# Kernel optimization log

Measured on AMD Instinct MI355X. Metric: run time of the kernel, lower is better.

## Reference

```python
import jax, jax.numpy as jnp
import numpy as np

# DPLayer config (init kwargs)
MAX_OP = False            # False -> min-plus (shortest path) semiring; null = +inf
MAKE_POS = True           # GraphLayer make_pos: force positive edge weights
NULL = -1e30 if MAX_OP else 1e30   # finite stand-in for +/-inf (grad-safe)
B, H, W = 512, 256, 256


def setup_inputs() -> dict:
    key = jax.random.key(0)
    images = jax.random.normal(key, (B, 1, H, W), dtype=jnp.float32)
    return {"images": images}


def _edge_weights(images):
    # GraphLayer: edge_f('euclidean') on pixel values, made positive via softplus.
    x = images[:, 0, :, :]                       # [B, H, W] node/edge costs theta
    if MAKE_POS:
        x = jax.nn.softplus(x)
    return x


def _dp(theta):
    # V[i,j] = theta[i,j] + comb(V[i-1,j], V[i-1,j-1], V[i,j-1]); comb = min (max_op=False)
    # Row recurrence is solved in parallel via prefix-sum + associative running-min:
    #   A[j] = comb(V[i-1,j], V[i-1,j-1])
    #   V[i,j] = S[j] + runmin_{k<=j}(A[k] - S[k-1]),  S = cumsum(theta row)
    comb = jnp.maximum if MAX_OP else jnp.minimum
    null = jnp.asarray(NULL, theta.dtype)
    b = theta.shape[0]

    v0 = jnp.cumsum(theta[:, 0, :], axis=-1)     # first row: only right moves

    def row_step(vprev, th_row):                 # vprev: [B,W], th_row: [B,W]
        shifted = jnp.concatenate([jnp.full((b, 1), null, theta.dtype), vprev[:, :-1]], axis=1)
        A = comb(vprev, shifted)                 # best of up / up-left
        S = jnp.cumsum(th_row, axis=-1)
        Sprev = jnp.concatenate([jnp.zeros((b, 1), theta.dtype), S[:, :-1]], axis=1)
        V = S + jax.lax.associative_scan(comb, A - Sprev, axis=-1)
        return V, None

    vlast, _ = jax.lax.scan(row_step, v0, jnp.moveaxis(theta[:, 1:, :], 1, 0))
    return vlast[:, -1]                          # path length to (H-1, W-1), [B]


def reference(images):
    theta = _edge_weights(images)
    fake_lengths = _dp(theta)
    return fake_lengths
```

## Files before the change

kernel.cpp:

```cpp
#include <hip/hip_runtime.h>


#define HH 256
#define WW 256
#define CH 32
#define NCH 8
#define NULLV 1e30f

#define SBAR() __builtin_amdgcn_sched_barrier(0)

template<int CTRL, int ROWM>
__device__ __forceinline__ float dpp_mov(float x, float oldv) {
    return __builtin_bit_cast(float, __builtin_amdgcn_update_dpp(
        __builtin_bit_cast(int, oldv), __builtin_bit_cast(int, x),
        CTRL, ROWM, 0xF, false));
}

__device__ __forceinline__ float wave_iscan_add(float x) {
    x += dpp_mov<0x111, 0xF>(x, 0.0f);
    x += dpp_mov<0x112, 0xF>(x, 0.0f);
    x += dpp_mov<0x114, 0xF>(x, 0.0f);
    x += dpp_mov<0x118, 0xF>(x, 0.0f);
    x += dpp_mov<0x142, 0xA>(x, 0.0f);
    x += dpp_mov<0x143, 0xC>(x, 0.0f);
    return x;
}

__device__ __forceinline__ float wave_iscan_min(float x) {
    x = fminf(x, dpp_mov<0x111, 0xF>(x, NULLV));
    x = fminf(x, dpp_mov<0x112, 0xF>(x, NULLV));
    x = fminf(x, dpp_mov<0x114, 0xF>(x, NULLV));
    x = fminf(x, dpp_mov<0x118, 0xF>(x, NULLV));
    x = fminf(x, dpp_mov<0x142, 0xA>(x, NULLV));
    x = fminf(x, dpp_mov<0x143, 0xC>(x, NULLV));
    return x;
}

__device__ __forceinline__ float softplus_f(float x) {
    float ax = fabsf(x);
    float t  = __expf(-ax);
    return fmaxf(x, 0.0f) + __logf(1.0f + t);
}

__device__ __forceinline__ float4 prep_row(float4 c) {
    float t0 = softplus_f(c.x);
    float t1 = t0 + softplus_f(c.y);
    float t2 = t1 + softplus_f(c.z);
    float t3 = t2 + softplus_f(c.w);
    float s    = wave_iscan_add(t3);
    float soff = dpp_mov<0x138, 0xF>(s, 0.0f);
    return make_float4(soff + t0, soff + t1, soff + t2, soff + t3);
}

template<int NR>
__device__ __forceinline__ void prep_run(const float4* gp, int row0,
                                         float* b0, float* b1, int lane) {
    float4 L[NR];
#pragma unroll
    for (int i = 0; i < NR; ++i) L[i] = gp[(size_t)(row0 + i) * 64];
    SBAR();
    for (int k = 0; k < NCH; ++k) {
        float4 N[NR];
#pragma unroll
        for (int i = 0; i < NR; ++i) N[i] = L[i];
        if (k + 1 < NCH) {
            const size_t rn = (size_t)(k + 1) * CH + row0;
#pragma unroll
            for (int i = 0; i < NR; ++i) N[i] = gp[(rn + i) * 64];
        }
        SBAR();
        float* buf = (k & 1) ? b1 : b0;
#pragma unroll
        for (int i = 0; i < NR; ++i)
            *reinterpret_cast<float4*>(&buf[i * WW + lane * 4]) = prep_row(L[i]);
        __syncthreads();
#pragma unroll
        for (int i = 0; i < NR; ++i) L[i] = N[i];
    }
}

__global__ __launch_bounds__(512, 1) void dp_kernel(const float* __restrict__ img,
                                                    float* __restrict__ out) {
    const int tid = threadIdx.x;
    const int wid = tid >> 6;
    const int lane = tid & 63;

    __shared__ __align__(16) float sbuf[2][2][CH][WW];

    if (wid < 2) {
        const int imgi = wid;
        __builtin_amdgcn_s_setprio(1);
        float v0, v1, v2, v3;

        auto row_step = [&](const float4& S) {
            float soff = dpp_mov<0x138, 0xF>(S.w, 0.0f);
            float vm1  = dpp_mov<0x138, 0xF>(v3, NULLV);
            float B0 = fminf(v0, vm1) - soff;
            float B1 = fminf(v1, v0) - S.x;
            float B2 = fminf(v2, v1) - S.y;
            float B3 = fminf(v3, v2) - S.z;
            float m1 = fminf(B0, B1);
            float m2 = fminf(m1, B2);
            float m3 = fminf(m2, B3);
            float mm   = wave_iscan_min(m3);
            float moff = dpp_mov<0x138, 0xF>(mm, NULLV);
            v0 = S.x + fminf(moff, B0);
            v1 = S.y + fminf(moff, m1);
            v2 = S.z + fminf(moff, m2);
            v3 = S.w + fminf(moff, m3);
        };

#define RD8(P, buf, r0)                                                  \
    P##0 = *reinterpret_cast<const float4*>(&(buf)[(r0) + 0][lane * 4]); \
    P##1 = *reinterpret_cast<const float4*>(&(buf)[(r0) + 1][lane * 4]); \
    P##2 = *reinterpret_cast<const float4*>(&(buf)[(r0) + 2][lane * 4]); \
    P##3 = *reinterpret_cast<const float4*>(&(buf)[(r0) + 3][lane * 4]); \
    P##4 = *reinterpret_cast<const float4*>(&(buf)[(r0) + 4][lane * 4]); \
    P##5 = *reinterpret_cast<const float4*>(&(buf)[(r0) + 5][lane * 4]); \
    P##6 = *reinterpret_cast<const float4*>(&(buf)[(r0) + 6][lane * 4]); \
    P##7 = *reinterpret_cast<const float4*>(&(buf)[(r0) + 7][lane * 4]);
#define ST8(P)                                                           \
    row_step(P##0); row_step(P##1); row_step(P##2); row_step(P##3);      \
    row_step(P##4); row_step(P##5); row_step(P##6); row_step(P##7);

        float4 A0, A1, A2, A3, A4, A5, A6, A7;
        float4 B0, B1, B2, B3, B4, B5, B6, B7;

        __syncthreads();
        {
            const float(*buf)[WW] = sbuf[imgi][0];
            RD8(A, buf, 0); RD8(B, buf, 8);
            v0 = A0.x; v1 = A0.y; v2 = A0.z; v3 = A0.w;
            row_step(A1); row_step(A2); row_step(A3);
            row_step(A4); row_step(A5); row_step(A6); row_step(A7);
            RD8(A, buf, 16);
            ST8(B);
            RD8(B, buf, 24);
            ST8(A);
            ST8(B);
        }
        for (int k = 1; k < NCH; ++k) {
            __syncthreads();
            const float(*buf)[WW] = sbuf[imgi][k & 1];
            RD8(A, buf, 0); RD8(B, buf, 8);
            ST8(A);
            RD8(A, buf, 16);
            ST8(B);
            RD8(B, buf, 24);
            ST8(A);
            ST8(B);
        }
#undef RD8
#undef ST8
        if (lane == 63) out[2 * blockIdx.x + imgi] = v3;
    } else {
        const int imgi = (wid - 2) & 1;
        const int pw   = (wid - 2) >> 1;
        const float* gbase = img + (size_t)(2 * blockIdx.x + imgi) * HH * WW;
        const float4* gp = reinterpret_cast<const float4*>(gbase) + lane;
        const int row0 = pw * 11;
        float* b0 = &sbuf[imgi][0][row0][0];
        float* b1 = &sbuf[imgi][1][row0][0];
        if (pw < 2) prep_run<11>(gp, row0, b0, b1, lane);
        else        prep_run<10>(gp, row0, b0, b1, lane);
    }
}

extern "C" void kernel_launch(void* const* d_in, const int* in_sizes, int n_in,
                              void* d_out, int out_size, void* d_ws, size_t ws_size,
                              hipStream_t stream) {
    const float* img = (const float*)d_in[0];
    float* out = (float*)d_out;
    dp_kernel<<<out_size / 2, 512, 0, stream>>>(img, out);
}
```

Measured before the change: 46.03 us.

## Shrink block to six waves and have DP waves prep first chunk

Reduces the block from 8 to 6 waves. The two DP waves now also load and softplus-prefix the first 11 rows of chunk 0 before starting the recurrence. The remaining four producer waves split the rest unevenly: 11 then 18 rows, and 10 then 14 rows per chunk. The row_step min-chain is rebalanced to shorten the dependency depth. The aim is to cut producer wave count and per-SIMD contention with the latency-critical DP waves. The cost is more registers per producer wave and possible producer stalls, since each producer now handles more rows per chunk.

```diff
diff --git a/kernel.cpp b/kernel.cpp
--- a/kernel.cpp
+++ b/kernel.cpp
@@ -6,8 +6,6 @@
 #define CH 32
 #define NCH 8
 #define NULLV 1e30f
-
-#define SBAR() __builtin_amdgcn_sched_barrier(0)
 
 template<int CTRL, int ROWM>
 __device__ __forceinline__ float dpp_mov(float x, float oldv) {
@@ -53,33 +51,19 @@
 }
 
 template<int NR>
-__device__ __forceinline__ void prep_run(const float4* gp, int row0,
-                                         float* b0, float* b1, int lane) {
-    float4 L[NR];
+__device__ __forceinline__ void load_rows(const float4* gp, int r0, float4* L) {
 #pragma unroll
-    for (int i = 0; i < NR; ++i) L[i] = gp[(size_t)(row0 + i) * 64];
-    SBAR();
-    for (int k = 0; k < NCH; ++k) {
-        float4 N[NR];
-#pragma unroll
-        for (int i = 0; i < NR; ++i) N[i] = L[i];
-        if (k + 1 < NCH) {
-            const size_t rn = (size_t)(k + 1) * CH + row0;
-#pragma unroll
-            for (int i = 0; i < NR; ++i) N[i] = gp[(rn + i) * 64];
-        }
-        SBAR();
-        float* buf = (k & 1) ? b1 : b0;
-#pragma unroll
-        for (int i = 0; i < NR; ++i)
-            *reinterpret_cast<float4*>(&buf[i * WW + lane * 4]) = prep_row(L[i]);
-        __syncthreads();
-#pragma unroll
-        for (int i = 0; i < NR; ++i) L[i] = N[i];
-    }
+    for (int i = 0; i < NR; ++i) L[i] = gp[(size_t)(r0 + i) * 64];
 }
 
-__global__ __launch_bounds__(512, 1) void dp_kernel(const float* __restrict__ img,
+template<int NR>
+__device__ __forceinline__ void prep_store(const float4* L, float* dst, int lane) {
+#pragma unroll
+    for (int i = 0; i < NR; ++i)
+        *reinterpret_cast<float4*>(&dst[i * WW + lane * 4]) = prep_row(L[i]);
+}
+
+__global__ __launch_bounds__(384, 1) void dp_kernel(const float* __restrict__ img,
                                                     float* __restrict__ out) {
     const int tid = threadIdx.x;
     const int wid = tid >> 6;
@@ -87,11 +71,20 @@
 
     __shared__ __align__(16) float sbuf[2][2][CH][WW];
 
+    const int imgi = wid & 1;
+    const float* gbase = img + (size_t)(2 * blockIdx.x + imgi) * HH * WW;
+    const float4* gp = reinterpret_cast<const float4*>(gbase) + lane;
+
     if (wid < 2) {
-        const int imgi = wid;
+        {
+            float4 C[11];
+            load_rows<11>(gp, 0, C);
+            prep_store<11>(C, &sbuf[imgi][0][0][0], lane);
+        }
+        __syncthreads();
         __builtin_amdgcn_s_setprio(1);
+
         float v0, v1, v2, v3;
-
         auto row_step = [&](const float4& S) {
             float soff = dpp_mov<0x138, 0xF>(S.w, 0.0f);
             float vm1  = dpp_mov<0x138, 0xF>(v3, NULLV);
@@ -100,8 +93,9 @@
             float B2 = fminf(v2, v1) - S.y;
             float B3 = fminf(v3, v2) - S.z;
             float m1 = fminf(B0, B1);
+            float p  = fminf(B2, B3);
             float m2 = fminf(m1, B2);
-            float m3 = fminf(m2, B3);
+            float m3 = fminf(m1, p);
             float mm   = wave_iscan_min(m3);
             float moff = dpp_mov<0x138, 0xF>(mm, NULLV);
             v0 = S.x + fminf(moff, B0);
@@ -126,7 +120,6 @@
         float4 A0, A1, A2, A3, A4, A5, A6, A7;
         float4 B0, B1, B2, B3, B4, B5, B6, B7;
 
-        __syncthreads();
         {
             const float(*buf)[WW] = sbuf[imgi][0];
             RD8(A, buf, 0); RD8(B, buf, 8);
@@ -153,16 +146,44 @@
 #undef RD8
 #undef ST8
         if (lane == 63) out[2 * blockIdx.x + imgi] = v3;
+    } else if (wid < 4) {
+        {
+            float4 C[11];
+            load_rows<11>(gp, 11, C);
+            prep_store<11>(C, &sbuf[imgi][0][11][0], lane);
+        }
+        float4 L[18];
+        load_rows<18>(gp, CH + 0, L);
+        __syncthreads();
+        for (int k = 1; k < NCH; ++k) {
+            float4 N[18];
+            if (k + 1 < NCH) load_rows<18>(gp, (k + 1) * CH + 0, N);
+            prep_store<18>(L, &sbuf[imgi][k & 1][0][0], lane);
+            __syncthreads();
+            if (k + 1 < NCH) {
+#pragma unroll
+                for (int i = 0; i < 18; ++i) L[i] = N[i];
+            }
+        }
     } else {
-        const int imgi = (wid - 2) & 1;
-        const int pw   = (wid - 2) >> 1;
-        const float* gbase = img + (size_t)(2 * blockIdx.x + imgi) * HH * WW;
-        const float4* gp = reinterpret_cast<const float4*>(gbase) + lane;
-        const int row0 = pw * 11;
-        float* b0 = &sbuf[imgi][0][row0][0];
-        float* b1 = &sbuf[imgi][1][row0][0];
-        if (pw < 2) prep_run<11>(gp, row0, b0, b1, lane);
-        else        prep_run<10>(gp, row0, b0, b1, lane);
+        {
+            float4 C[10];
+            load_rows<10>(gp, 22, C);
+            prep_store<10>(C, &sbuf[imgi][0][22][0], lane);
+        }
+        float4 L[14];
+        load_rows<14>(gp, CH + 18, L);
+        __syncthreads();
+        for (int k = 1; k < NCH; ++k) {
+            float4 N[14];
+            if (k + 1 < NCH) load_rows<14>(gp, (k + 1) * CH + 18, N);
+            prep_store<14>(L, &sbuf[imgi][k & 1][18][0], lane);
+            __syncthreads();
+            if (k + 1 < NCH) {
+#pragma unroll
+                for (int i = 0; i < 14; ++i) L[i] = N[i];
+            }
+        }
     }
 }
 
@@ -171,5 +192,5 @@
                               hipStream_t stream) {
     const float* img = (const float*)d_in[0];
     float* out = (float*)d_out;
-    dp_kernel<<<out_size / 2, 512, 0, stream>>>(img, out);
+    dp_kernel<<<out_size / 2, 384, 0, stream>>>(img, out);
 }
```

After: 55.50 us. 1.21x slower.

## Halve chunk size and let scan waves help prep the first chunk

Applied to the files above, without the earlier changes.

Chunks shrink from 32 to 16 rows, so the LDS double buffer is half the size and twice as many chunks are handed over, which shortens the initial pipeline fill. The first chunk is split across all eight waves, with the two scan waves also loading and transforming four rows each, so the serial DP can start sooner. The per-row min chain is also rebalanced into a shallower tree. The cost is twice as many block-wide barriers, which may add synchronisation stalls on the latency-critical scan waves.

```diff
diff --git a/kernel.cpp b/kernel.cpp
--- a/kernel.cpp
+++ b/kernel.cpp
@@ -3,11 +3,9 @@
 
 #define HH 256
 #define WW 256
-#define CH 32
-#define NCH 8
+#define CH 16
+#define NCH 16
 #define NULLV 1e30f
-
-#define SBAR() __builtin_amdgcn_sched_barrier(0)
 
 template<int CTRL, int ROWM>
 __device__ __forceinline__ float dpp_mov(float x, float oldv) {
@@ -53,29 +51,33 @@
 }
 
 template<int NR>
+__device__ __forceinline__ void load_rows(const float4* gp, int r0, float4* L) {
+#pragma unroll
+    for (int i = 0; i < NR; ++i) L[i] = gp[(size_t)(r0 + i) * 64];
+}
+
+template<int NR>
+__device__ __forceinline__ void prep_store(const float4* L, float* dst, int lane) {
+#pragma unroll
+    for (int i = 0; i < NR; ++i)
+        *reinterpret_cast<float4*>(&dst[i * WW + lane * 4]) = prep_row(L[i]);
+}
+
+template<int NR>
 __device__ __forceinline__ void prep_run(const float4* gp, int row0,
-                                         float* b0, float* b1, int lane) {
+                                         float* base0, float* base1, int lane) {
     float4 L[NR];
+    load_rows<NR>(gp, CH + row0, L);
+    __syncthreads();
+    for (int k = 1; k < NCH; ++k) {
+        float4 N[NR];
+        if (k + 1 < NCH) load_rows<NR>(gp, (k + 1) * CH + row0, N);
+        prep_store<NR>(L, (k & 1) ? base1 : base0, lane);
+        __syncthreads();
+        if (k + 1 < NCH) {
 #pragma unroll
-    for (int i = 0; i < NR; ++i) L[i] = gp[(size_t)(row0 + i) * 64];
-    SBAR();
-    for (int k = 0; k < NCH; ++k) {
-        float4 N[NR];
-#pragma unroll
-        for (int i = 0; i < NR; ++i) N[i] = L[i];
-        if (k + 1 < NCH) {
-            const size_t rn = (size_t)(k + 1) * CH + row0;
-#pragma unroll
-            for (int i = 0; i < NR; ++i) N[i] = gp[(rn + i) * 64];
+            for (int i = 0; i < NR; ++i) L[i] = N[i];
         }
-        SBAR();
-        float* buf = (k & 1) ? b1 : b0;
-#pragma unroll
-        for (int i = 0; i < NR; ++i)
-            *reinterpret_cast<float4*>(&buf[i * WW + lane * 4]) = prep_row(L[i]);
-        __syncthreads();
-#pragma unroll
-        for (int i = 0; i < NR; ++i) L[i] = N[i];
     }
 }
 
@@ -87,11 +89,20 @@
 
     __shared__ __align__(16) float sbuf[2][2][CH][WW];
 
+    const int imgi = (wid < 2) ? wid : ((wid - 2) & 1);
+    const float* gbase = img + (size_t)(2 * blockIdx.x + imgi) * HH * WW;
+    const float4* gp = reinterpret_cast<const float4*>(gbase) + lane;
+
     if (wid < 2) {
-        const int imgi = wid;
+        {
+            float4 C[4];
+            load_rows<4>(gp, 0, C);
+            prep_store<4>(C, &sbuf[imgi][0][0][0], lane);
+        }
+        __syncthreads();
         __builtin_amdgcn_s_setprio(1);
+
         float v0, v1, v2, v3;
-
         auto row_step = [&](const float4& S) {
             float soff = dpp_mov<0x138, 0xF>(S.w, 0.0f);
             float vm1  = dpp_mov<0x138, 0xF>(v3, NULLV);
@@ -100,8 +111,9 @@
             float B2 = fminf(v2, v1) - S.y;
             float B3 = fminf(v3, v2) - S.z;
             float m1 = fminf(B0, B1);
+            float p  = fminf(B2, B3);
             float m2 = fminf(m1, B2);
-            float m3 = fminf(m2, B3);
+            float m3 = fminf(m1, p);
             float mm   = wave_iscan_min(m3);
             float moff = dpp_mov<0x138, 0xF>(mm, NULLV);
             v0 = S.x + fminf(moff, B0);
@@ -126,17 +138,12 @@
         float4 A0, A1, A2, A3, A4, A5, A6, A7;
         float4 B0, B1, B2, B3, B4, B5, B6, B7;
 
-        __syncthreads();
         {
             const float(*buf)[WW] = sbuf[imgi][0];
             RD8(A, buf, 0); RD8(B, buf, 8);
             v0 = A0.x; v1 = A0.y; v2 = A0.z; v3 = A0.w;
             row_step(A1); row_step(A2); row_step(A3);
             row_step(A4); row_step(A5); row_step(A6); row_step(A7);
-            RD8(A, buf, 16);
-            ST8(B);
-            RD8(B, buf, 24);
-            ST8(A);
             ST8(B);
         }
         for (int k = 1; k < NCH; ++k) {
@@ -144,25 +151,23 @@
             const float(*buf)[WW] = sbuf[imgi][k & 1];
             RD8(A, buf, 0); RD8(B, buf, 8);
             ST8(A);
-            RD8(A, buf, 16);
-            ST8(B);
-            RD8(B, buf, 24);
-            ST8(A);
             ST8(B);
         }
 #undef RD8
 #undef ST8
         if (lane == 63) out[2 * blockIdx.x + imgi] = v3;
     } else {
-        const int imgi = (wid - 2) & 1;
-        const int pw   = (wid - 2) >> 1;
-        const float* gbase = img + (size_t)(2 * blockIdx.x + imgi) * HH * WW;
-        const float4* gp = reinterpret_cast<const float4*>(gbase) + lane;
-        const int row0 = pw * 11;
+        const int pw = (wid - 2) >> 1;
+        {
+            float4 C[4];
+            load_rows<4>(gp, 4 + 4 * pw, C);
+            prep_store<4>(C, &sbuf[imgi][0][4 + 4 * pw][0], lane);
+        }
+        const int row0 = (pw == 0) ? 0 : (pw == 1) ? 6 : 11;
         float* b0 = &sbuf[imgi][0][row0][0];
         float* b1 = &sbuf[imgi][1][row0][0];
-        if (pw < 2) prep_run<11>(gp, row0, b0, b1, lane);
-        else        prep_run<10>(gp, row0, b0, b1, lane);
+        if (pw == 0) prep_run<6>(gp, row0, b0, b1, lane);
+        else         prep_run<5>(gp, row0, b0, b1, lane);
     }
 }
 
```

Result: no change. 46.18 us (+0.3%).
